# Kernel tuning notes

Hardware: AMD Instinct MI355X
Metric: run time of the kernel (lower is better)

Reference implementation:

```python
import jax, jax.numpy as jnp
import numpy as np

L, N, E, H, K = 2048, 8, 2048, 8192, 8

def setup_inputs() -> dict:
    key = jax.random.key(0)
    ks = jax.random.split(key, 6)
    return {
        'x': jax.random.normal(ks[0], (L, N, E), dtype=jnp.float32),
        'proj1': jax.random.normal(ks[1], (H, E), dtype=jnp.float32) * 0.02,
        'proj1_bias': jax.random.normal(ks[2], (H,), dtype=jnp.float32) * 0.02,
        'proj2': jax.random.normal(ks[3], (E, H), dtype=jnp.float32) * 0.02,
        'proj2_bias': jax.random.normal(ks[4], (E,), dtype=jnp.float32) * 0.02,
        'gate_w': jax.random.normal(ks[5], (E, K), dtype=jnp.float32),
    }

def reference(x, proj1, proj1_bias, proj2, proj2_bias, gate_w):
    # Gating: top-1 expert per token (argmax over expert affinities).
    # NOTE: in the source, every expert applies the SAME shared proj1/proj2,
    # and recv_from_experts restores the original token order exactly, so the
    # dispatch/combine is a mathematical identity permutation. The forward
    # math is therefore exactly a shared two-layer GELU MLP on all tokens.
    dst = jnp.argmax(jnp.einsum('lne,ek->lnk', x, gate_w), axis=-1)  # [L,N] int, routing ids
    h = jax.nn.gelu(jnp.einsum('lne,he->lnh', x, proj1) + proj1_bias, approximate=False)
    out = jnp.einsum('lnh,eh->lne', h, proj2) + proj2_bias
    del dst  # routing does not affect the output (shared expert weights)
    return out
```

## Files before the change

kernel.cpp:

```cpp
#include <hip/hip_runtime.h>
#include <hip/hip_bf16.h>
#include <cstdint>
#include <cstddef>

typedef __bf16 bf16_t;
typedef __bf16 bf16x4 __attribute__((ext_vector_type(4)));
typedef __bf16 bf16x8 __attribute__((ext_vector_type(8)));
typedef float  f32x4  __attribute__((ext_vector_type(4)));

#define L_DIM 2048
#define N_DIM 8
#define E_DIM 2048
#define H_DIM 8192
#define T_DIM (L_DIM * N_DIM)

__global__ __launch_bounds__(256) void cvt_f32_bf16(const float* __restrict__ in,
                                                    bf16_t* __restrict__ out,
                                                    int n4) {
    int stride = gridDim.x * blockDim.x;
    for (int i = blockIdx.x * blockDim.x + threadIdx.x; i < n4; i += stride) {
        float4 v = *(const float4*)(in + (size_t)i * 4);
        bf16x4 o;
        o[0] = (bf16_t)v.x; o[1] = (bf16_t)v.y;
        o[2] = (bf16_t)v.z; o[3] = (bf16_t)v.w;
        *(bf16x4*)(out + (size_t)i * 4) = o;
    }
}

__device__ __forceinline__ float fast_gelu(float x) {
    float x2 = x * x;
    float w  = x * __builtin_fmaf(0.1029456f, x2, 2.3022618f);
    w = fminf(w, 60.0f);
    float s = __builtin_amdgcn_exp2f(w);
    float r = __builtin_amdgcn_rcpf(s + 1.0f);
    return x * s * r;
}

template <bool GELU_OUT, int LG_NT, int LG_TN, int LG_NTILE, int KDIM, int NDIM>
__global__ __launch_bounds__(512, 2) void gemm256(const bf16_t* __restrict__ Am,
                                                  const bf16_t* __restrict__ Bm,
                                                  const float* __restrict__ bias,
                                                  void* __restrict__ Cout) {
    extern __shared__ char lds[];
    constexpr int NT    = 1 << LG_NT;
    constexpr int ntile = 1 << LG_NTILE;
    constexpr int U     = ntile << LG_NT;

    const int tid  = threadIdx.x;
    const int lane = tid & 63;
    const int wid  = tid >> 6;
    const int wr   = wid >> 2;
    const int wc   = wid & 3;

    const int wgb = (blockIdx.x & 7) * 32 + (blockIdx.x >> 3);

    const int srow  = wid * 8 + (lane >> 3);
    const int scol8 = ((lane & 7) ^ (lane >> 3)) * 8;

    auto STAGE = [&](int isB, int half, int slot) {
        const int us  = (slot < U) ? slot : (U - 1);
        const int ti_ = us >> LG_NT;
        const int kt_ = us & (NT - 1);
        const int g_  = (wgb << LG_NTILE) + ti_;
        const size_t base_ = (size_t)(isB ? (g_ & ((1 << LG_TN) - 1)) : (g_ >> LG_TN)) << 8;
        const unsigned reg_ = (unsigned)(((slot & 1) << 16) | (isB << 15) | (half << 14));
        const bf16_t* s0 = (isB ? Bm : Am)
                         + (base_ + (size_t)(half * 128 + srow)) * (size_t)KDIM
                         + (size_t)((kt_ << 6) + scol8);
        __builtin_amdgcn_global_load_lds(
            (const __attribute__((address_space(1))) void*)s0,
            (__attribute__((address_space(3))) void*)(lds + reg_ + (unsigned)(wid * 1024)),
            16, 0, 0);
        __builtin_amdgcn_global_load_lds(
            (const __attribute__((address_space(1))) void*)(s0 + (size_t)64 * KDIM),
            (__attribute__((address_space(3))) void*)(lds + reg_ + (unsigned)((8 + wid) * 1024)),
            16, 0, 0);
    };

    auto ldsA = [&](unsigned bufo, int m, int kk) -> bf16x8 {
        const int row  = (m >> 1) * 64 + wr * 32 + (m & 1) * 16 + (lane & 15);
        const int slot = ((kk << 2) + (lane >> 4)) ^ (lane & 7);
        return *(const bf16x8*)(lds + bufo + row * 128 + slot * 16);
    };
    auto ldsB = [&](unsigned bufo, int n, int kk) -> bf16x8 {
        const int row  = wc * 64 + n * 16 + (lane & 15);
        const int slot = ((kk << 2) + (lane >> 4)) ^ (lane & 7);
        return *(const bf16x8*)(lds + bufo + 32768 + row * 128 + slot * 16);
    };

    f32x4 acc[8][4] = {};

    STAGE(1, 0, 0); STAGE(1, 1, 0); STAGE(0, 0, 0); STAGE(0, 1, 0);
    STAGE(1, 0, 1); STAGE(1, 1, 1); STAGE(0, 0, 1);
    asm volatile("s_waitcnt vmcnt(6)" ::: "memory");
    __builtin_amdgcn_s_barrier();

    for (int ti = 0; ti < ntile; ++ti) {
        for (int t = 0; t < NT; ++t) {
            const int u = (ti << LG_NT) + t;
            const unsigned cur = (unsigned)(t & 1) * 65536u;
            bf16x8 bf[4][2];
            bf16x8 af[2][2];

#pragma unroll
            for (int n = 0; n < 4; ++n)
#pragma unroll
                for (int kk = 0; kk < 2; ++kk)
                    bf[n][kk] = ldsB(cur, n, kk);
#pragma unroll
            for (int mm = 0; mm < 2; ++mm)
#pragma unroll
                for (int kk = 0; kk < 2; ++kk)
                    af[mm][kk] = ldsA(cur, mm, kk);
            STAGE(0, 1, u + 1);
            asm volatile("s_waitcnt lgkmcnt(8)" ::: "memory");
            __builtin_amdgcn_s_barrier();
            asm volatile("s_waitcnt lgkmcnt(0)" ::: "memory");
            __builtin_amdgcn_s_setprio(1);
#pragma unroll
            for (int mm = 0; mm < 2; ++mm)
#pragma unroll
                for (int n = 0; n < 4; ++n)
#pragma unroll
                    for (int kk = 0; kk < 2; ++kk)
                        acc[mm][n] = __builtin_amdgcn_mfma_f32_16x16x32_bf16(
                            af[mm][kk], bf[n][kk], acc[mm][n], 0, 0, 0);
            __builtin_amdgcn_s_setprio(0);
            __builtin_amdgcn_s_barrier();

#pragma unroll
            for (int ph = 1; ph < 4; ++ph) {
#pragma unroll
                for (int mm = 0; mm < 2; ++mm)
#pragma unroll
                    for (int kk = 0; kk < 2; ++kk)
                        af[mm][kk] = ldsA(cur, ph * 2 + mm, kk);
                if (ph == 1)      STAGE(1, 0, u + 2);
                else if (ph == 2) STAGE(1, 1, u + 2);
                else {            STAGE(0, 0, u + 2);
                                  asm volatile("s_waitcnt vmcnt(6)" ::: "memory"); }
                __builtin_amdgcn_s_barrier();
                asm volatile("s_waitcnt lgkmcnt(0)" ::: "memory");
                __builtin_amdgcn_s_setprio(1);
#pragma unroll
                for (int mm = 0; mm < 2; ++mm)
#pragma unroll
                    for (int n = 0; n < 4; ++n)
#pragma unroll
                        for (int kk = 0; kk < 2; ++kk)
                            acc[ph * 2 + mm][n] = __builtin_amdgcn_mfma_f32_16x16x32_bf16(
                                af[mm][kk], bf[n][kk], acc[ph * 2 + mm][n], 0, 0, 0);
                __builtin_amdgcn_s_setprio(0);
                __builtin_amdgcn_s_barrier();
            }
        }

        const int g = (wgb << LG_NTILE) + ti;
        const size_t rowBase = (size_t)(g >> LG_TN) << 8;
        const size_t colBase = (size_t)(g & ((1 << LG_TN) - 1)) << 8;
        const int orow = (lane >> 4) * 4;
        const int ocol = lane & 15;
#pragma unroll
        for (int m = 0; m < 8; ++m) {
            const size_t rb = rowBase + (size_t)((m >> 1) * 64 + wr * 32 + (m & 1) * 16 + orow);
#pragma unroll
            for (int n = 0; n < 4; ++n) {
                const size_t col = colBase + (size_t)(wc * 64 + n * 16 + ocol);
                const float bv = bias[col];
#pragma unroll
                for (int j = 0; j < 4; ++j) {
                    float v = acc[m][n][j] + bv;
                    if constexpr (GELU_OUT) {
                        ((bf16_t*)Cout)[(rb + j) * (size_t)NDIM + col] = (bf16_t)fast_gelu(v);
                    } else {
                        ((float*)Cout)[(rb + j) * (size_t)NDIM + col] = v;
                    }
                }
                acc[m][n] = (f32x4){0.f, 0.f, 0.f, 0.f};
            }
        }
    }
    asm volatile("s_waitcnt vmcnt(0)" ::: "memory");
}

extern "C" void kernel_launch(void* const* d_in, const int* in_sizes, int n_in,
                              void* d_out, int out_size, void* d_ws, size_t ws_size,
                              hipStream_t stream) {
    const float* x  = (const float*)d_in[0];
    const float* p1 = (const float*)d_in[1];
    const float* b1 = (const float*)d_in[2];
    const float* p2 = (const float*)d_in[3];
    const float* b2 = (const float*)d_in[4];
    float* out = (float*)d_out;

    char* ws = (char*)d_ws;
    bf16_t* xb  = (bf16_t*)(ws);
    bf16_t* p1b = (bf16_t*)(ws + ((size_t)64 << 20));
    bf16_t* p2b = (bf16_t*)(ws + ((size_t)96 << 20));
    bf16_t* h   = (bf16_t*)(ws + ((size_t)128 << 20));

    auto g1 = gemm256<true, 5, 5, 3, E_DIM, H_DIM>;
    auto g2 = gemm256<false, 7, 3, 1, H_DIM, E_DIM>;

    (void)hipFuncSetAttribute((const void*)g1,
                              hipFuncAttributeMaxDynamicSharedMemorySize, 131072);
    (void)hipFuncSetAttribute((const void*)g2,
                              hipFuncAttributeMaxDynamicSharedMemorySize, 131072);

    cvt_f32_bf16<<<2048, 256, 0, stream>>>(x,  xb,  (T_DIM * E_DIM) / 4);
    cvt_f32_bf16<<<1024, 256, 0, stream>>>(p1, p1b, (H_DIM * E_DIM) / 4);
    cvt_f32_bf16<<<1024, 256, 0, stream>>>(p2, p2b, (E_DIM * H_DIM) / 4);

    g1<<<256, 512, 131072, stream>>>(xb, p1b, b1, (void*)h);
    g2<<<256, 512, 131072, stream>>>(h, p2b, b2, (void*)out);
}
```

Measured before the change: 1.055 ms.

## Software-pipeline LDS fragment reads ahead of MFMA phases with double-buffered registers

Restructures the GEMM main loop so the LDS reads for the next phase's A fragments, and the next k-tile's B fragments, are issued before the current phase's MFMAs. Two B fragment register sets and two A fragment sets alternate across phases. Each phase now uses one barrier instead of two, and LDS read addresses are precomputed as per-lane offsets, which cuts address arithmetic. In exchange it uses more registers, which could hurt occupancy at launch bounds of 512 threads with 2 blocks, and the waitcnt and barrier ordering is tighter and easier to get wrong.

Result: slower. 1.220 ms (+15.7%).

```diff
diff --git a/kernel.cpp b/kernel.cpp
--- a/kernel.cpp
+++ b/kernel.cpp
@@ -44,7 +44,6 @@
     extern __shared__ char lds[];
     constexpr int NT    = 1 << LG_NT;
     constexpr int ntile = 1 << LG_NTILE;
-    constexpr int U     = ntile << LG_NT;
 
     const int tid  = threadIdx.x;
     const int lane = tid & 63;
@@ -53,109 +52,122 @@
     const int wc   = wid & 3;
 
     const int wgb = (blockIdx.x & 7) * 32 + (blockIdx.x >> 3);
-
-    const int srow  = wid * 8 + (lane >> 3);
-    const int scol8 = ((lane & 7) ^ (lane >> 3)) * 8;
-
-    auto STAGE = [&](int isB, int half, int slot) {
-        const int us  = (slot < U) ? slot : (U - 1);
-        const int ti_ = us >> LG_NT;
-        const int kt_ = us & (NT - 1);
-        const int g_  = (wgb << LG_NTILE) + ti_;
-        const size_t base_ = (size_t)(isB ? (g_ & ((1 << LG_TN) - 1)) : (g_ >> LG_TN)) << 8;
-        const unsigned reg_ = (unsigned)(((slot & 1) << 16) | (isB << 15) | (half << 14));
-        const bf16_t* s0 = (isB ? Bm : Am)
-                         + (base_ + (size_t)(half * 128 + srow)) * (size_t)KDIM
-                         + (size_t)((kt_ << 6) + scol8);
-        __builtin_amdgcn_global_load_lds(
-            (const __attribute__((address_space(1))) void*)s0,
-            (__attribute__((address_space(3))) void*)(lds + reg_ + (unsigned)(wid * 1024)),
-            16, 0, 0);
-        __builtin_amdgcn_global_load_lds(
-            (const __attribute__((address_space(1))) void*)(s0 + (size_t)64 * KDIM),
-            (__attribute__((address_space(3))) void*)(lds + reg_ + (unsigned)((8 + wid) * 1024)),
-            16, 0, 0);
-    };
-
-    auto ldsA = [&](unsigned bufo, int m, int kk) -> bf16x8 {
-        const int row  = (m >> 1) * 64 + wr * 32 + (m & 1) * 16 + (lane & 15);
-        const int slot = ((kk << 2) + (lane >> 4)) ^ (lane & 7);
-        return *(const bf16x8*)(lds + bufo + row * 128 + slot * 16);
-    };
-    auto ldsB = [&](unsigned bufo, int n, int kk) -> bf16x8 {
-        const int row  = wc * 64 + n * 16 + (lane & 15);
-        const int slot = ((kk << 2) + (lane >> 4)) ^ (lane & 7);
-        return *(const bf16x8*)(lds + bufo + 32768 + row * 128 + slot * 16);
-    };
-
-    f32x4 acc[8][4] = {};
-
-    STAGE(1, 0, 0); STAGE(1, 1, 0); STAGE(0, 0, 0); STAGE(0, 1, 0);
-    STAGE(1, 0, 1); STAGE(1, 1, 1); STAGE(0, 0, 1);
+    const int g0  = wgb << LG_NTILE;
+
+    const int srow    = wid * 8 + (lane >> 3);
+    const int scol8   = ((lane & 7) ^ (lane >> 3)) * 8;
+    const int laneOff = srow * KDIM + scol8;
+
+    const int l15 = lane & 15;
+    const int sl0 = ((lane >> 4)    ) ^ (lane & 7);
+    const int sl1 = (4 + (lane >> 4)) ^ (lane & 7);
+    const unsigned rdA0_0 = (unsigned)((wr * 32 + l15) * 128 + sl0 * 16);
+    const unsigned rdA1_0 = (unsigned)((wr * 32 + l15) * 128 + sl1 * 16);
+    const unsigned rdB0_0 = (unsigned)(32768 + (wc * 64 + l15) * 128 + sl0 * 16);
+    const unsigned rdB1_0 = (unsigned)(32768 + (wc * 64 + l15) * 128 + sl1 * 16);
+    const unsigned rdA0_1 = rdA0_0 + 65536u;
+    const unsigned rdA1_1 = rdA1_0 + 65536u;
+    const unsigned rdB0_1 = rdB0_0 + 65536u;
+    const unsigned rdB1_1 = rdB1_0 + 65536u;
+
+#define LDA(P, M, KK) (*(const bf16x8*)(lds + ((KK) ? ((P) ? rdA1_1 : rdA1_0)      \
+                                                    : ((P) ? rdA0_1 : rdA0_0))      \
+                                            + ((M) >> 1) * 8192 + ((M) & 1) * 2048))
+#define LDB(P, N, KK) (*(const bf16x8*)(lds + ((KK) ? ((P) ? rdB1_1 : rdB1_0)      \
+                                                    : ((P) ? rdB0_1 : rdB0_0))      \
+                                            + (N) * 2048))
+#define RD_A(dst, P, M0) do {                                                       \
+        dst[0][0] = LDA(P, (M0),     0); dst[0][1] = LDA(P, (M0),     1);           \
+        dst[1][0] = LDA(P, (M0) + 1, 0); dst[1][1] = LDA(P, (M0) + 1, 1); } while (0)
+#define RD_B(dst, P) do {                                                           \
+        dst[0][0] = LDB(P, 0, 0); dst[0][1] = LDB(P, 0, 1);                         \
+        dst[1][0] = LDB(P, 1, 0); dst[1][1] = LDB(P, 1, 1);                         \
+        dst[2][0] = LDB(P, 2, 0); dst[2][1] = LDB(P, 2, 1);                         \
+        dst[3][0] = LDB(P, 3, 0); dst[3][1] = LDB(P, 3, 1); } while (0)
+
+#define GLL(src, dofs)                                                              \
+    __builtin_amdgcn_global_load_lds(                                               \
+        (const __attribute__((address_space(1))) void*)(src),                       \
+        (__attribute__((address_space(3))) void*)(lds + (dofs)), 16, 0, 0)
+
+#define STAGE(BASE, ISB, HALF, PARL, KT) do {                                       \
+        const bf16_t* s0_ = (BASE) + (size_t)(HALF) * 128 * KDIM + laneOff          \
+                          + ((KT) << 6);                                            \
+        const unsigned d_ = ((unsigned)((PARL) << 16) | ((unsigned)(ISB) << 15)     \
+                          | ((unsigned)(HALF) << 14)) | ((unsigned)wid << 10);      \
+        GLL(s0_, d_);                                                               \
+        GLL(s0_ + (size_t)64 * KDIM, d_ + 8192); } while (0)
+
+#define MFMA16(AB, AF, BF) do {                                                     \
+        _Pragma("unroll") for (int mm = 0; mm < 2; ++mm)                            \
+        _Pragma("unroll") for (int n = 0; n < 4; ++n)                               \
+        _Pragma("unroll") for (int kk = 0; kk < 2; ++kk)                            \
+            acc[(AB) + mm][n] = __builtin_amdgcn_mfma_f32_16x16x32_bf16(            \
+                AF[mm][kk], BF[n][kk], acc[(AB) + mm][n], 0, 0, 0); } while (0)
+
+#define PH_MID(LGKM)                                                                \
+        __builtin_amdgcn_sched_barrier(0);                                          \
+        asm volatile("s_waitcnt lgkmcnt(" #LGKM ")" ::: "memory");                  \
+        __builtin_amdgcn_sched_barrier(0);                                          \
+        __builtin_amdgcn_s_setprio(1);
+#define PH_END                                                                      \
+        __builtin_amdgcn_s_setprio(0);                                              \
+        asm volatile("s_waitcnt vmcnt(6)" ::: "memory");                            \
+        __builtin_amdgcn_s_barrier();
+
+#define KITER(T_, BC, BN, PAR) do {                                                 \
+        const int t_  = (T_);                                                       \
+        const int kt1 = (t_ + 1) & (NT - 1);                                        \
+        const int kt2 = (t_ + 2) & (NT - 1);                                        \
+        const bool nx1 = (t_ == NT - 1);                                            \
+        const bool nx2 = (t_ >= NT - 2);                                            \
+                              \
+        RD_A(afY, PAR, 2);                                                          \
+        STAGE(nx1 ? aNxt : aCur, 0, 1, (PAR) ^ 1, kt1);                             \
+        PH_MID(4)  MFMA16(0, afX, BC); PH_END                                       \
+                              \
+        RD_A(afX, PAR, 4);                                                          \
+        STAGE(nx2 ? bNxt : bCur, 1, 0, PAR, kt2);                                   \
+        PH_MID(4)  MFMA16(2, afY, BC); PH_END                                       \
+                     \
+        RD_A(afY, PAR, 6);                                                          \
+        RD_B(BN, (PAR) ^ 1);                                                        \
+        STAGE(nx2 ? bNxt : bCur, 1, 1, PAR, kt2);                                   \
+        PH_MID(12) MFMA16(4, afX, BC); PH_END                                       \
+                            \
+        RD_A(afX, (PAR) ^ 1, 0);                                                    \
+        STAGE(nx2 ? aNxt : aCur, 0, 0, PAR, kt2);                                   \
+        PH_MID(12) MFMA16(6, afY, BC); PH_END                                       \
+    } while (0)
+
+    const bf16_t* aCur = Am + ((size_t)(g0 >> LG_TN) << 8) * KDIM;
+    const bf16_t* bCur = Bm + ((size_t)(g0 & ((1 << LG_TN) - 1)) << 8) * KDIM;
+    const bf16_t* aNxt = aCur;
+    const bf16_t* bNxt = bCur;
+
+    f32x4  acc[8][4] = {};
+    bf16x8 bfA[4][2], bfB[4][2], afX[2][2], afY[2][2];
+
+    STAGE(bCur, 1, 0, 0, 0); STAGE(bCur, 1, 1, 0, 0);
+    STAGE(aCur, 0, 0, 0, 0); STAGE(aCur, 0, 1, 0, 0);
+    STAGE(bCur, 1, 0, 1, 1); STAGE(bCur, 1, 1, 1, 1);
+    STAGE(aCur, 0, 0, 1, 1);
     asm volatile("s_waitcnt vmcnt(6)" ::: "memory");
     __builtin_amdgcn_s_barrier();
+    RD_B(bfA, 0);
+    RD_A(afX, 0, 0);
 
     for (int ti = 0; ti < ntile; ++ti) {
-        for (int t = 0; t < NT; ++t) {
-            const int u = (ti << LG_NT) + t;
-            const unsigned cur = (unsigned)(t & 1) * 65536u;
-            bf16x8 bf[4][2];
-            bf16x8 af[2][2];
-
-#pragma unroll
-            for (int n = 0; n < 4; ++n)
-#pragma unroll
-                for (int kk = 0; kk < 2; ++kk)
-                    bf[n][kk] = ldsB(cur, n, kk);
-#pragma unroll
-            for (int mm = 0; mm < 2; ++mm)
-#pragma unroll
-                for (int kk = 0; kk < 2; ++kk)
-                    af[mm][kk] = ldsA(cur, mm, kk);
-            STAGE(0, 1, u + 1);
-            asm volatile("s_waitcnt lgkmcnt(8)" ::: "memory");
-            __builtin_amdgcn_s_barrier();
-            asm volatile("s_waitcnt lgkmcnt(0)" ::: "memory");
-            __builtin_amdgcn_s_setprio(1);
-#pragma unroll
-            for (int mm = 0; mm < 2; ++mm)
-#pragma unroll
-                for (int n = 0; n < 4; ++n)
-#pragma unroll
-                    for (int kk = 0; kk < 2; ++kk)
-                        acc[mm][n] = __builtin_amdgcn_mfma_f32_16x16x32_bf16(
-                            af[mm][kk], bf[n][kk], acc[mm][n], 0, 0, 0);
-            __builtin_amdgcn_s_setprio(0);
-            __builtin_amdgcn_s_barrier();
-
-#pragma unroll
-            for (int ph = 1; ph < 4; ++ph) {
-#pragma unroll
-                for (int mm = 0; mm < 2; ++mm)
-#pragma unroll
-                    for (int kk = 0; kk < 2; ++kk)
-                        af[mm][kk] = ldsA(cur, ph * 2 + mm, kk);
-                if (ph == 1)      STAGE(1, 0, u + 2);
-                else if (ph == 2) STAGE(1, 1, u + 2);
-                else {            STAGE(0, 0, u + 2);
-                                  asm volatile("s_waitcnt vmcnt(6)" ::: "memory"); }
-                __builtin_amdgcn_s_barrier();
-                asm volatile("s_waitcnt lgkmcnt(0)" ::: "memory");
-                __builtin_amdgcn_s_setprio(1);
-#pragma unroll
-                for (int mm = 0; mm < 2; ++mm)
-#pragma unroll
-                    for (int n = 0; n < 4; ++n)
-#pragma unroll
-                        for (int kk = 0; kk < 2; ++kk)
-                            acc[ph * 2 + mm][n] = __builtin_amdgcn_mfma_f32_16x16x32_bf16(
-                                af[mm][kk], bf[n][kk], acc[ph * 2 + mm][n], 0, 0, 0);
-                __builtin_amdgcn_s_setprio(0);
-                __builtin_amdgcn_s_barrier();
-            }
+        const int gn = (ti < ntile - 1) ? (g0 + ti + 1) : (g0 + ntile - 1);
+        aNxt = Am + ((size_t)(gn >> LG_TN) << 8) * KDIM;
+        bNxt = Bm + ((size_t)(gn & ((1 << LG_TN) - 1)) << 8) * KDIM;
+
+        for (int t = 0; t < NT; t += 2) {
+            KITER(t,     bfA, bfB, 0);
+            KITER(t + 1, bfB, bfA, 1);
         }
 
-        const int g = (wgb << LG_NTILE) + ti;
+        const int g = g0 + ti;
         const size_t rowBase = (size_t)(g >> LG_TN) << 8;
         const size_t colBase = (size_t)(g & ((1 << LG_TN) - 1)) << 8;
         const int orow = (lane >> 4) * 4;
@@ -179,8 +191,21 @@
                 acc[m][n] = (f32x4){0.f, 0.f, 0.f, 0.f};
             }
         }
+
+        aCur = aNxt; bCur = bNxt;
     }
     asm volatile("s_waitcnt vmcnt(0)" ::: "memory");
+
+#undef KITER
+#undef PH_END
+#undef PH_MID
+#undef MFMA16
+#undef STAGE
+#undef GLL
+#undef RD_B
+#undef RD_A
+#undef LDB
+#undef LDA
 }
 
 extern "C" void kernel_launch(void* const* d_in, const int* in_sizes, int n_in,
```

## Restructure GEMM main loop to single-step prefetch with fewer barriers

Applied to the files above, without the earlier changes.

Replaces the staggered two-tiles-ahead global-to-LDS prefetch with a one-tile-ahead schedule. Each of the four compute phases now issues one quarter of the next tile's loads. The trailing barrier after every MFMA phase is removed, and explicit vmcnt waits are placed at phases 1 and 3, cutting synchronization overhead. The trade-off is less time to hide global-load latency, plus a possible LDS write-after-read hazard on the alternate buffer now that the end-of-phase barriers are gone.

After: 1.019 ms. 1.03x faster.

```diff
diff --git a/kernel.cpp b/kernel.cpp
--- a/kernel.cpp
+++ b/kernel.cpp
@@ -53,6 +53,7 @@
     const int wc   = wid & 3;
 
     const int wgb = (blockIdx.x & 7) * 32 + (blockIdx.x >> 3);
+    const int g0  = wgb << LG_NTILE;
 
     const int srow  = wid * 8 + (lane >> 3);
     const int scol8 = ((lane & 7) ^ (lane >> 3)) * 8;
@@ -61,7 +62,7 @@
         const int us  = (slot < U) ? slot : (U - 1);
         const int ti_ = us >> LG_NT;
         const int kt_ = us & (NT - 1);
-        const int g_  = (wgb << LG_NTILE) + ti_;
+        const int g_  = g0 + ti_;
         const size_t base_ = (size_t)(isB ? (g_ & ((1 << LG_TN) - 1)) : (g_ >> LG_TN)) << 8;
         const unsigned reg_ = (unsigned)(((slot & 1) << 16) | (isB << 15) | (half << 14));
         const bf16_t* s0 = (isB ? Bm : Am)
@@ -91,8 +92,7 @@
     f32x4 acc[8][4] = {};
 
     STAGE(1, 0, 0); STAGE(1, 1, 0); STAGE(0, 0, 0); STAGE(0, 1, 0);
-    STAGE(1, 0, 1); STAGE(1, 1, 1); STAGE(0, 0, 1);
-    asm volatile("s_waitcnt vmcnt(6)" ::: "memory");
+    asm volatile("s_waitcnt vmcnt(0)" ::: "memory");
     __builtin_amdgcn_s_barrier();
 
     for (int ti = 0; ti < ntile; ++ti) {
@@ -102,6 +102,7 @@
             bf16x8 bf[4][2];
             bf16x8 af[2][2];
 
+            STAGE(1, 0, u + 1);
 #pragma unroll
             for (int n = 0; n < 4; ++n)
 #pragma unroll
@@ -112,8 +113,6 @@
 #pragma unroll
                 for (int kk = 0; kk < 2; ++kk)
                     af[mm][kk] = ldsA(cur, mm, kk);
-            STAGE(0, 1, u + 1);
-            asm volatile("s_waitcnt lgkmcnt(8)" ::: "memory");
             __builtin_amdgcn_s_barrier();
             asm volatile("s_waitcnt lgkmcnt(0)" ::: "memory");
             __builtin_amdgcn_s_setprio(1);
@@ -126,36 +125,68 @@
                         acc[mm][n] = __builtin_amdgcn_mfma_f32_16x16x32_bf16(
                             af[mm][kk], bf[n][kk], acc[mm][n], 0, 0, 0);
             __builtin_amdgcn_s_setprio(0);
-            __builtin_amdgcn_s_barrier();
-
-#pragma unroll
-            for (int ph = 1; ph < 4; ++ph) {
-#pragma unroll
-                for (int mm = 0; mm < 2; ++mm)
-#pragma unroll
-                    for (int kk = 0; kk < 2; ++kk)
-                        af[mm][kk] = ldsA(cur, ph * 2 + mm, kk);
-                if (ph == 1)      STAGE(1, 0, u + 2);
-                else if (ph == 2) STAGE(1, 1, u + 2);
-                else {            STAGE(0, 0, u + 2);
-                                  asm volatile("s_waitcnt vmcnt(6)" ::: "memory"); }
-                __builtin_amdgcn_s_barrier();
-                asm volatile("s_waitcnt lgkmcnt(0)" ::: "memory");
-                __builtin_amdgcn_s_setprio(1);
-#pragma unroll
-                for (int mm = 0; mm < 2; ++mm)
-#pragma unroll
-                    for (int n = 0; n < 4; ++n)
-#pragma unroll
-                        for (int kk = 0; kk < 2; ++kk)
-                            acc[ph * 2 + mm][n] = __builtin_amdgcn_mfma_f32_16x16x32_bf16(
-                                af[mm][kk], bf[n][kk], acc[ph * 2 + mm][n], 0, 0, 0);
-                __builtin_amdgcn_s_setprio(0);
-                __builtin_amdgcn_s_barrier();
-            }
+
+            STAGE(1, 1, u + 1);
+#pragma unroll
+            for (int mm = 0; mm < 2; ++mm)
+#pragma unroll
+                for (int kk = 0; kk < 2; ++kk)
+                    af[mm][kk] = ldsA(cur, 2 + mm, kk);
+            asm volatile("s_waitcnt vmcnt(4)" ::: "memory");
+            __builtin_amdgcn_s_barrier();
+            asm volatile("s_waitcnt lgkmcnt(0)" ::: "memory");
+            __builtin_amdgcn_s_setprio(1);
+#pragma unroll
+            for (int mm = 0; mm < 2; ++mm)
+#pragma unroll
+                for (int n = 0; n < 4; ++n)
+#pragma unroll
+                    for (int kk = 0; kk < 2; ++kk)
+                        acc[2 + mm][n] = __builtin_amdgcn_mfma_f32_16x16x32_bf16(
+                            af[mm][kk], bf[n][kk], acc[2 + mm][n], 0, 0, 0);
+            __builtin_amdgcn_s_setprio(0);
+
+            STAGE(0, 0, u + 1);
+#pragma unroll
+            for (int mm = 0; mm < 2; ++mm)
+#pragma unroll
+                for (int kk = 0; kk < 2; ++kk)
+                    af[mm][kk] = ldsA(cur, 4 + mm, kk);
+            __builtin_amdgcn_s_barrier();
+            asm volatile("s_waitcnt lgkmcnt(0)" ::: "memory");
+            __builtin_amdgcn_s_setprio(1);
+#pragma unroll
+            for (int mm = 0; mm < 2; ++mm)
+#pragma unroll
+                for (int n = 0; n < 4; ++n)
+#pragma unroll
+                    for (int kk = 0; kk < 2; ++kk)
+                        acc[4 + mm][n] = __builtin_amdgcn_mfma_f32_16x16x32_bf16(
+                            af[mm][kk], bf[n][kk], acc[4 + mm][n], 0, 0, 0);
+            __builtin_amdgcn_s_setprio(0);
+
+            STAGE(0, 1, u + 1);
+#pragma unroll
+            for (int mm = 0; mm < 2; ++mm)
+#pragma unroll
+                for (int kk = 0; kk < 2; ++kk)
+                    af[mm][kk] = ldsA(cur, 6 + mm, kk);
+            asm volatile("s_waitcnt vmcnt(2)" ::: "memory");
+            __builtin_amdgcn_s_barrier();
+            asm volatile("s_waitcnt lgkmcnt(0)" ::: "memory");
+            __builtin_amdgcn_s_setprio(1);
+#pragma unroll
+            for (int mm = 0; mm < 2; ++mm)
+#pragma unroll
+                for (int n = 0; n < 4; ++n)
+#pragma unroll
+                    for (int kk = 0; kk < 2; ++kk)
+                        acc[6 + mm][n] = __builtin_amdgcn_mfma_f32_16x16x32_bf16(
+                            af[mm][kk], bf[n][kk], acc[6 + mm][n], 0, 0, 0);
+            __builtin_amdgcn_s_setprio(0);
         }
 
-        const int g = (wgb << LG_NTILE) + ti;
+        const int g = g0 + ti;
         const size_t rowBase = (size_t)(g >> LG_TN) << 8;
         const size_t colBase = (size_t)(g & ((1 << LG_TN) - 1)) << 8;
         const int orow = (lane >> 4) * 4;
```
